# Kernel tuning notes

Hardware: AMD Instinct MI355X
Metric: run time of the kernel (lower is better)

The kernel has to match this reference:

```python
import jax, jax.numpy as jnp
import numpy as np

N, E, H = 25000, 100000, 32          # nodes, edges, node/clique hidden dim
NC, A, EC = 8000, 50000, 24000       # cliques, node2clique assignments, clique edges
EEMB, CEE, L = 8, 8, 2               # edge emb dims, n layers


def segment_mean(vals, ids, num):
    s = jax.ops.segment_sum(vals, ids, num_segments=num)
    cnt = jax.ops.segment_sum(jnp.ones(ids.shape[0], vals.dtype), ids, num_segments=num)
    return s / jnp.maximum(cnt, 1.0)[:, None]


def setup_inputs() -> dict:
    key = jax.random.key(0)
    ks = jax.random.split(key, 24)
    s = 0.1  # param scale
    inp = {
        "node_features": jax.random.normal(ks[0], (N, H), jnp.float32),
        "edge_index": jax.random.randint(ks[1], (2, E), 0, N),
        "edge_features": jax.random.normal(ks[2], (E, EEMB), jnp.float32),
        "clique_features": jax.random.normal(ks[3], (NC, H), jnp.float32),
        "node2clique_index": jnp.stack([
            jax.random.randint(ks[4], (A,), 0, N),
            jax.random.randint(ks[5], (A,), 0, NC)]),
        "clique_edge_index": jax.random.randint(ks[6], (2, EC), 0, NC),
        "clique_edge_features": jax.random.normal(ks[7], (EC, CEE), jnp.float32),
        # node NNConv params (stacked over L layers)
        "nn1_w": jax.random.normal(ks[8], (L, EEMB, H)) * s,
        "nn1_b": jnp.zeros((L, H)),
        "nn2_w": jax.random.normal(ks[9], (L, H, H * H)) * s,
        "nn2_b": jnp.zeros((L, H * H)),
        "root_w": jax.random.normal(ks[10], (L, H, H)) * s,
        "root_b": jnp.zeros((L, H)),
        # Node2Clique linear
        "n2c_w": jax.random.normal(ks[11], (L, H, H)) * s,
        "n2c_b": jnp.zeros((L, H)),
        # clique NNConv params
        "cnn1_w": jax.random.normal(ks[12], (L, CEE, H)) * s,
        "cnn1_b": jnp.zeros((L, H)),
        "cnn2_w": jax.random.normal(ks[13], (L, H, H * H)) * s,
        "cnn2_b": jnp.zeros((L, H * H)),
        "croot_w": jax.random.normal(ks[14], (L, H, H)) * s,
        "croot_b": jnp.zeros((L, H)),
        # Clique2Node linear
        "c2n_w": jax.random.normal(ks[15], (L, H, H)) * s,
        "c2n_b": jnp.zeros((L, H)),
    }
    return inp


def nnconv(x, src, dst, edge_attr, w1, b1, w2, b2, rw, rb, n_out_nodes):
    # per-edge weight matrices from the edge MLP: [E, in, out]
    h = jax.nn.relu(edge_attr @ w1 + b1)
    We = (h @ w2 + b2).reshape(edge_attr.shape[0], x.shape[1], -1)
    msg = jnp.einsum('ei,eio->eo', x[src], We)           # message from source
    agg = segment_mean(msg, dst, n_out_nodes)            # mean aggregation at target
    return agg + x @ rw + rb                             # root weight + bias


def reference(node_features, edge_index, edge_features, clique_features,
              node2clique_index, clique_edge_index, clique_edge_features,
              nn1_w, nn1_b, nn2_w, nn2_b, root_w, root_b, n2c_w, n2c_b,
              cnn1_w, cnn1_b, cnn2_w, cnn2_b, croot_w, croot_b, c2n_w, c2n_b):
    x, c = node_features, clique_features
    src, dst = edge_index[0], edge_index[1]
    nid, cid = node2clique_index[0], node2clique_index[1]
    csrc, cdst = clique_edge_index[0], clique_edge_index[1]
    for l in range(L):
        # node-level edge-conditioned conv
        x = jax.nn.relu(nnconv(x, src, dst, edge_features,
                               nn1_w[l], nn1_b[l], nn2_w[l], nn2_b[l],
                               root_w[l], root_b[l], N))
        # Node2Clique: project node feats, scatter-mean into cliques
        m = x @ n2c_w[l] + n2c_b[l]
        c = c + segment_mean(m[nid], cid, NC)
        # clique-level edge-conditioned conv
        c = jax.nn.relu(nnconv(c, csrc, cdst, clique_edge_features,
                               cnn1_w[l], cnn1_b[l], cnn2_w[l], cnn2_b[l],
                               croot_w[l], croot_b[l], NC))
        # Clique2Node: project clique feats, scatter-mean back onto nodes
        m = c @ c2n_w[l] + c2n_b[l]
        x = x + segment_mean(m[cid], nid, N)
    return (x, c)
```

## Files before the change

kernel.cpp:

```cpp
#include <hip/hip_runtime.h>
#include <hip/hip_bf16.h>

typedef unsigned int u32;
typedef unsigned short u16;

#define DEVINL __device__ __forceinline__

constexpr int Nn  = 25000;
constexpr int Ee  = 100000;
constexpr int NCc = 8000;
constexpr int Aa  = 50000;
constexpr int ECc = 24000;
constexpr int TCOLS = 1088;
constexpr int WPSZ  = TCOLS*32;
constexpr int TT_ROW = 561;
constexpr int NB_N = (Nn + 255)/256;
constexpr int NB_C = (NCc + 255)/256;
constexpr int PB_EN = (Ee + 255)/256;
constexpr int PB_EC = (ECc + 255)/256;
constexpr int PB_AS = (2*Aa + 255)/256;
constexpr int PB_WP = (4*WPSZ + 255)/256;

typedef float f32x4 __attribute__((ext_vector_type(4)));
typedef _Float16 h16x2 __attribute__((ext_vector_type(2)));
typedef _Float16 h16x8 __attribute__((ext_vector_type(8)));

DEVINL float b2f(u16 u){ union{u32 i;float f;}v; v.i = ((u32)u)<<16; return v.f; }
DEVINL float bfl(u32 u){ union{u32 i;float f;}v; v.i = u<<16; return v.f; }
DEVINL float bfh(u32 u){ union{u32 i;float f;}v; v.i = u & 0xffff0000u; return v.f; }
DEVINL u16 f2b(float f){ union{float f;u32 i;}v; v.f=f; u32 i=v.i;
  return (u16)((i + 0x7fffu + ((i>>16)&1u)) >> 16); }
DEVINL u16 f2h(float x){ union{ _Float16 h; u16 u; } v; v.h = (_Float16)x; return v.u; }
DEVINL u32 pkh2(float a, float b){
  union{ _Float16 h[2]; u32 u; } v;
  v.h[0] = (_Float16)a; v.h[1] = (_Float16)b; return v.u;
}
DEVINL float ldw(const void* p, long i, int f){
  return f ? ((const float*)p)[i] : b2f(((const u16*)p)[i]);
}
DEVINL float dot2f(u32 a, u32 b, float c){
  union U{u32 u; h16x2 h;};
  U ua; ua.u = a; U ub; ub.u = b;
#if __has_builtin(__builtin_amdgcn_fdot2)
  return __builtin_amdgcn_fdot2(ua.h, ub.h, c, false);
#else
  return c + (float)ua.h[0]*(float)ub.h[0] + (float)ua.h[1]*(float)ub.h[1];
#endif
}

__global__ __launch_bounds__(256) void k_detect_count(const u16* __restrict__ p, int n,
                        u32* __restrict__ maxbits, int* __restrict__ zcnt,
                        int* __restrict__ done, int* __restrict__ flag,
                        const int* __restrict__ ei, const int* __restrict__ cei,
                        const int* __restrict__ n2c,
                        int* __restrict__ deg_nd, int* __restrict__ deg_ce,
                        int* __restrict__ deg_n2c, int* __restrict__ deg_c2n,
                        int* __restrict__ cnt_sn, int* __restrict__ cnt_sc){
  int i0 = blockIdx.x*256 + threadIdx.x;
  { int t = i0;
    if (t < Ee)                             atomicAdd(&deg_nd[ei[Ee + t]], 1);
    else if ((t -= Ee) < ECc)               atomicAdd(&deg_ce[cei[ECc + t]], 1);
    else if ((t -= ECc) < Aa)               atomicAdd(&deg_n2c[n2c[Aa + t]], 1);
    else if ((t -= Aa) < Aa)                atomicAdd(&deg_c2n[n2c[t]], 1);
    else if ((t -= Aa) < Ee)                atomicAdd(&cnt_sn[ei[t]], 1);
    else if ((t -= Ee) < ECc)               atomicAdd(&cnt_sc[cei[t]], 1);
  }
  if (blockIdx.x >= 256) return;
  float lm = 0.f; int lz = 0;
  for (int i = i0; i < n; i += 256*256){
    u16 v = p[i];
    if (v == 0) lz++;
    lm = fmaxf(lm, fabsf(b2f(v)));
  }
  #pragma unroll
  for (int off = 32; off; off >>= 1){
    lm = fmaxf(lm, __shfl_down(lm, off));
    lz += __shfl_down(lz, off);
  }
  __shared__ float smax[4]; __shared__ int szc[4];
  if ((threadIdx.x & 63) == 0){
    smax[threadIdx.x >> 6] = lm;
    szc[threadIdx.x >> 6] = lz;
  }
  __syncthreads();
  if (threadIdx.x == 0){
    float m = fmaxf(fmaxf(smax[0], smax[1]), fmaxf(smax[2], smax[3]));
    int z = szc[0] + szc[1] + szc[2] + szc[3];
    atomicMax(maxbits, __float_as_uint(m));
    atomicAdd(zcnt, z);
    __threadfence();
    if (atomicAdd(done, 1) == 255){
      float mm = __uint_as_float(*maxbits);
      *flag = (mm > 1e6f || *zcnt > n/4) ? 1 : 0;
    }
  }
}

DEVINL void segof(int bid, int& seg, int& rb){
  seg = 0; rb = bid;
  while (true){
    int nb = (seg & 1) ? NB_C : NB_N;
    if (rb < nb) break;
    rb -= nb; seg++;
  }
}

__global__ __launch_bounds__(256) void k_scan_block6(
    const int* __restrict__ c0, const int* __restrict__ c1,
    const int* __restrict__ c2, const int* __restrict__ c3,
    const int* __restrict__ c4, const int* __restrict__ c5,
    int* __restrict__ o0, int* __restrict__ o1, int* __restrict__ o2,
    int* __restrict__ o3, int* __restrict__ o4, int* __restrict__ o5,
    int* __restrict__ b0, int* __restrict__ b1, int* __restrict__ b2,
    int* __restrict__ b3, int* __restrict__ b4, int* __restrict__ b5){
  __shared__ int s[256];
  int seg, rb; segof(blockIdx.x, seg, rb);
  const int* cnt; int* offs; int* bs;
  switch (seg){
    case 0: cnt=c0; offs=o0; bs=b0; break;
    case 1: cnt=c1; offs=o1; bs=b1; break;
    case 2: cnt=c2; offs=o2; bs=b2; break;
    case 3: cnt=c3; offs=o3; bs=b3; break;
    case 4: cnt=c4; offs=o4; bs=b4; break;
    default: cnt=c5; offs=o5; bs=b5; break;
  }
  int M = (seg & 1) ? NCc : Nn;
  int tid = threadIdx.x;
  int i = rb*256 + tid;
  int v = (i < M) ? cnt[i] : 0;
  s[tid] = v; __syncthreads();
  for (int d = 1; d < 256; d <<= 1){
    int t = (tid >= d) ? s[tid-d] : 0;
    __syncthreads();
    s[tid] += t;
    __syncthreads();
  }
  if (i < M) offs[i] = s[tid] - v;
  if (tid == 255) bs[rb] = s[255];
}

__global__ __launch_bounds__(256) void k_scan_fix6(
    int* __restrict__ o0, int* __restrict__ o1, int* __restrict__ o2,
    int* __restrict__ o3, int* __restrict__ o4, int* __restrict__ o5,
    const int* __restrict__ b0, const int* __restrict__ b1, const int* __restrict__ b2,
    const int* __restrict__ b3, const int* __restrict__ b4, const int* __restrict__ b5){
  __shared__ int s[256];
  int seg, rb; segof(blockIdx.x, seg, rb);
  int* offs; const int* bsp;
  switch (seg){
    case 0: offs=o0; bsp=b0; break;
    case 1: offs=o1; bsp=b1; break;
    case 2: offs=o2; bsp=b2; break;
    case 3: offs=o3; bsp=b3; break;
    case 4: offs=o4; bsp=b4; break;
    default: offs=o5; bsp=b5; break;
  }
  int M = (seg & 1) ? NCc : Nn;
  int tid = threadIdx.x;
  int v = (tid < rb) ? bsp[tid] : 0;
  s[tid] = v; __syncthreads();
  #pragma unroll
  for (int d = 128; d; d >>= 1){
    if (tid < d) s[tid] += s[tid + d];
    __syncthreads();
  }
  int prefix = s[0];
  int i = rb*256 + tid;
  if (i < M) offs[i] += prefix;
}

__global__ __launch_bounds__(256) void k_place_pack(
    const int* __restrict__ ei, const int* __restrict__ cei, const int* __restrict__ n2c,
    const void* __restrict__ ef, const void* __restrict__ cef,
    const void* __restrict__ nn1w, const void* __restrict__ nn1b,
    const void* __restrict__ cnn1w, const void* __restrict__ cnn1b,
    const void* __restrict__ nn2w, const void* __restrict__ nn2b, const void* __restrict__ rootw,
    const void* __restrict__ cnn2w, const void* __restrict__ cnn2b, const void* __restrict__ crootw,
    const int* __restrict__ offs_n, const int* __restrict__ offs_c,
    const int* __restrict__ offs_an, const int* __restrict__ offs_ac,
    const int* __restrict__ doffs_n, const int* __restrict__ doffs_c,
    int* __restrict__ cur_n, int* __restrict__ cur_c,
    int* __restrict__ cur_an, int* __restrict__ cur_ac,
    int* __restrict__ cur_dn, int* __restrict__ cur_dc,
    int2* __restrict__ sdp_n, int2* __restrict__ sdp_c,
    u32* __restrict__ hp_n, u32* __restrict__ hp_c,
    int* __restrict__ an2c, int* __restrict__ ac2n,
    const int* __restrict__ flag, u16* __restrict__ Wp4){
  int b = blockIdx.x, tid = threadIdx.x;
  int f = *flag;
  if (b < PB_EN + PB_EC){
    __shared__ float w1s[2][256], b1s[2][32];
    int isC = (b >= PB_EN);
    int e = (isC ? b - PB_EN : b)*256 + tid;
    int E = isC ? ECc : Ee;
    const void* W1 = isC ? cnn1w : nn1w;
    const void* B1 = isC ? cnn1b : nn1b;
    w1s[0][tid] = ldw(W1, tid, f);
    w1s[1][tid] = ldw(W1, 256 + tid, f);
    if (tid < 32){ b1s[0][tid] = ldw(B1, tid, f); b1s[1][tid] = ldw(B1, 32 + tid, f); }
    __syncthreads();
    if (e < E){
      const int* EI = isC ? cei : ei;
      int s = EI[e], d = EI[E + e];
      int* cur = isC ? cur_c : cur_n;
      const int* offs = isC ? offs_c : offs_n;
      int p = offs[s] + atomicAdd(&cur[s], 1);
      const int* dofs = isC ? doffs_c : doffs_n;
      int* curd = isC ? cur_dc : cur_dn;
      int dsl = dofs[d] + atomicAdd(&curd[d], 1);
      (isC ? sdp_c : sdp_n)[p] = make_int2(s, dsl);
      const void* EF = isC ? cef : ef;
      float ev[8];
      #pragma unroll
      for (int j = 0; j < 8; j++) ev[j] = ldw(EF, (long)e*8 + j, f);
      u32* hp = isC ? hp_c : hp_n;
      #pragma unroll
      for (int l = 0; l < 2; l++){
        u32* hq = hp + (size_t)l*E*16 + (size_t)p*16;
        #pragma unroll
        for (int kk = 0; kk < 16; kk++){
          float a0 = b1s[l][2*kk], a1 = b1s[l][2*kk+1];
          #pragma unroll
          for (int j = 0; j < 8; j++){
            a0 += ev[j]*w1s[l][j*32 + 2*kk];
            a1 += ev[j]*w1s[l][j*32 + 2*kk + 1];
          }
          hq[kk] = pkh2(fmaxf(a0, 0.f), fmaxf(a1, 0.f));
        }
      }
    }
  } else if (b < PB_EN + PB_EC + PB_AS){
    int i = (b - PB_EN - PB_EC)*256 + tid;
    if (i < Aa){
      int c = n2c[Aa + i];
      an2c[offs_ac[c] + atomicAdd(&cur_ac[c], 1)] = n2c[i];
    } else if ((i -= Aa) < Aa){
      int nd = n2c[i];
      ac2n[offs_an[nd] + atomicAdd(&cur_an[nd], 1)] = n2c[Aa + i];
    }
  } else {
    int i = (b - PB_EN - PB_EC - PB_AS)*256 + tid;
    if (i >= 4*WPSZ) return;
    int set = i / WPSZ, j = i - set*WPSZ;
    int l = set >> 1, isC = set & 1;
    const void* W2 = isC ? cnn2w : nn2w;
    const void* B2 = isC ? cnn2b : nn2b;
    const void* RW = isC ? crootw : rootw;
    int col = j >> 5, ii = j & 31;
    float v;
    if (col < 1024)      v = ldw(W2, (long)l*32768 + ((col>>5)<<10) + (ii<<5) + (col&31), f);
    else if (col < 1056) v = ldw(B2, (long)l*1024 + (ii<<5) + (col-1024), f);
    else                 v = ldw(RW, (long)l*1024 + (ii<<5) + (col-1056), f);
    Wp4[i] = f2h(v);
  }
}

__global__ __launch_bounds__(512) void k_conv_fused(const void* __restrict__ base, int braw,
                           const float* __restrict__ adm, const int* __restrict__ sidx,
                           const int* __restrict__ soffs, const int* __restrict__ sdeg, int M,
                           const int2* __restrict__ sdp, const u32* __restrict__ hp,
                           const int* __restrict__ offs, int E_,
                           const u16* __restrict__ Wp,
                           const void* __restrict__ rb, long rboff,
                           const int* __restrict__ flag,
                           float* __restrict__ feat_root, float* __restrict__ msg){
  __shared__ __align__(16) u32 Tt[16*TT_ROW];
  __shared__ __align__(16) u32 hws[8][64];
  int tid = threadIdx.x;
  int w = tid >> 6, lane = tid & 63;
  int quad = lane >> 4, lm = lane & 15;
  int n0 = blockIdx.x * 16;
  int f = *flag;
  int n = n0 + lm;
  int nc = n < M ? n : M-1;
  long bidx = (long)nc*32 + quad*8;
  float fv[8];
  if (braw && f == 0){
    uint4 q = *(const uint4*)((const u16*)base + bidx);
    fv[0]=bfl(q.x); fv[1]=bfh(q.x); fv[2]=bfl(q.y); fv[3]=bfh(q.y);
    fv[4]=bfl(q.z); fv[5]=bfh(q.z); fv[6]=bfl(q.w); fv[7]=bfh(q.w);
  } else {
    const float4* bp = (const float4*)((const float*)base + bidx);
    float4 q0 = bp[0], q1 = bp[1];
    fv[0]=q0.x; fv[1]=q0.y; fv[2]=q0.z; fv[3]=q0.w;
    fv[4]=q1.x; fv[5]=q1.y; fv[6]=q1.z; fv[7]=q1.w;
  }
  if (adm){
    int slo = soffs[nc], scnt = sdeg[nc];
    float ac[8] = {0,0,0,0,0,0,0,0};
    for (int k = 0; k < scnt; k++){
      const float4* mp = (const float4*)(adm + (size_t)sidx[slo + k]*32 + quad*8);
      float4 a0 = mp[0], a1 = mp[1];
      ac[0]+=a0.x; ac[1]+=a0.y; ac[2]+=a0.z; ac[3]+=a0.w;
      ac[4]+=a1.x; ac[5]+=a1.y; ac[6]+=a1.z; ac[7]+=a1.w;
    }
    float inv = 1.f/(float)(scnt > 1 ? scnt : 1);
    #pragma unroll
    for (int j = 0; j < 8; j++) fv[j] += ac[j]*inv;
  }
  union { h16x8 v; u32 u[4]; } bf;
  #pragma unroll
  for (int j = 0; j < 4; j++) bf.u[j] = pkh2(fv[2*j], fv[2*j+1]);

  #define AFR(ct) (*(const h16x8*)(Wp + (size_t)((ct)*16 + lm)*32 + quad*8))
  f32x4 z4 = {0.f, 0.f, 0.f, 0.f};
  #pragma unroll
  for (int g = 0; g < 2; g++){
    int q = w + 8*g;
    f32x4 c0 = __builtin_amdgcn_mfma_f32_16x16x32_f16(AFR(4*q+0), bf.v, z4, 0, 0, 0);
    f32x4 c1 = __builtin_amdgcn_mfma_f32_16x16x32_f16(AFR(4*q+1), bf.v, z4, 0, 0, 0);
    f32x4 c2 = __builtin_amdgcn_mfma_f32_16x16x32_f16(AFR(4*q+2), bf.v, z4, 0, 0, 0);
    f32x4 c3 = __builtin_amdgcn_mfma_f32_16x16x32_f16(AFR(4*q+3), bf.v, z4, 0, 0, 0);
    int rbase = lm*TT_ROW;
    int ob = quad*4;
    #pragma unroll
    for (int i = 0; i < 4; i++){
      Tt[rbase + (ob+i)*17 + q]      = pkh2(c0[i], c2[i]);
      Tt[rbase + (16+ob+i)*17 + q]   = pkh2(c1[i], c3[i]);
    }
  }
  if (w < 4){
    int ct = 64 + w;
    f32x4 c = __builtin_amdgcn_mfma_f32_16x16x32_f16(AFR(ct), bf.v, z4, 0, 0, 0);
    if (ct < 66){
      int p0 = (ct-64)*8 + quad*2;
      Tt[lm*TT_ROW + 544 + p0]     = pkh2(c[0], c[1]);
      Tt[lm*TT_ROW + 544 + p0 + 1] = pkh2(c[2], c[3]);
    } else if (n < M){
      int o = (ct-66)*16 + quad*4;
      float4 v = make_float4(c[0] + ldw(rb, rboff+o,   f),
                             c[1] + ldw(rb, rboff+o+1, f),
                             c[2] + ldw(rb, rboff+o+2, f),
                             c[3] + ldw(rb, rboff+o+3, f));
      *(float4*)&feat_root[(size_t)n*32 + o] = v;
    }
  }
  __syncthreads();

  int lo = offs[n0];
  int hi = (n0 + 16 < M) ? offs[n0 + 16] : E_;
  int eg = quad, kk = lm;
  int pos = lo + w*4;
  u32 hp0 = 0, hp1 = 0; int sd0 = 0, sd1 = 0;
  { int idx = pos*16 + lane;      if (idx < hi*16) hp0 = hp[idx];
    idx = (pos+32)*16 + lane;     if (idx < hi*16) hp1 = hp[idx]; }
  if (lane < 8){
    int idx = pos*2 + lane;       if (idx < hi*2) sd0 = ((const int*)sdp)[idx];
    idx = (pos+32)*2 + lane;      if (idx < hi*2) sd1 = ((const int*)sdp)[idx];
  }
  for (; pos < hi; pos += 32){
    int np = pos + 64;
    u32 hp2 = 0; int sd2 = 0;
    { int idx = np*16 + lane; if (idx < hi*16) hp2 = hp[idx]; }
    if (lane < 8){ int idx = np*2 + lane; if (idx < hi*2) sd2 = ((const int*)sdp)[idx]; }
    hws[w][lane] = hp0;
    int sn = __shfl(sd0, 2*eg);
    int ds = __shfl(sd0, 2*eg + 1);
    bool valid = (pos + eg < hi);
    int sr = sn - n0; sr = sr < 0 ? 0 : (sr > 15 ? 15 : sr);
    const u32* Tr = Tt + sr*TT_ROW;
    const u32* T0 = Tr + 34*kk;
    const uint4* Hp4 = (const uint4*)&hws[w][eg*16];
    union{u32 u; h16x2 h;} b2u; b2u.u = Tr[544 + kk];
    float m0 = (float)b2u.h[0], m1 = (float)b2u.h[1];
    #pragma unroll
    for (int g = 0; g < 4; g++){
      uint4 hv4 = Hp4[g];
      m0 = dot2f(hv4.x, T0[4*g+0], m0);  m1 = dot2f(hv4.x, T0[17+4*g+0], m1);
      m0 = dot2f(hv4.y, T0[4*g+1], m0);  m1 = dot2f(hv4.y, T0[17+4*g+1], m1);
      m0 = dot2f(hv4.z, T0[4*g+2], m0);  m1 = dot2f(hv4.z, T0[17+4*g+2], m1);
      m0 = dot2f(hv4.w, T0[4*g+3], m0);  m1 = dot2f(hv4.w, T0[17+4*g+3], m1);
    }
    if (valid){
      float* ap = msg + (size_t)ds*32 + 2*kk;
      ap[0] = m0;
      ap[1] = m1;
    }
    hp0 = hp1; sd0 = sd1; hp1 = hp2; sd1 = sd2;
  }
  #undef AFR
}

__global__ __launch_bounds__(256) void k_update_lin(const float* __restrict__ msg,
                           const int* __restrict__ doffs, const int* __restrict__ deg,
                           const float* __restrict__ feat_root, int M,
                           const void* __restrict__ w, long woff,
                           const void* __restrict__ b, long boff,
                           const int* __restrict__ flag,
                           float* __restrict__ feat, float* __restrict__ mout){
  __shared__ float wsm[1024], bs[32], rows[8][33];
  int tid = threadIdx.x;
  int f = *flag;
  for (int idx = tid; idx < 1024; idx += 256) wsm[idx] = ldw(w, woff + idx, f);
  if (tid < 32) bs[tid] = ldw(b, boff + tid, f);
  int nl = tid >> 5, o = tid & 31;
  int n = blockIdx.x*8 + nl;
  long i = (long)n*32 + o;
  if (n < M){
    int lo = doffs[n], dg = deg[n];
    float a = 0.f;
    for (int k = 0; k < dg; k++) a += msg[(size_t)(lo + k)*32 + o];
    float d = (float)(dg > 1 ? dg : 1);
    float v = fmaxf(a/d + feat_root[i], 0.f);
    rows[nl][o] = v;
    feat[i] = v;
  }
  __syncthreads();
  if (n >= M) return;
  float acc = bs[o];
  #pragma unroll
  for (int j = 0; j < 32; j++) acc += rows[nl][j]*wsm[j*32+o];
  mout[i] = acc;
}

__global__ __launch_bounds__(256) void k_store(const float* __restrict__ x,
                      const float* __restrict__ mC, const int* __restrict__ sidx,
                      const int* __restrict__ soffs, const int* __restrict__ sdeg,
                      const float* __restrict__ c,
                      void* __restrict__ out, const int* __restrict__ flag){
  int i = blockIdx.x*256 + threadIdx.x;
  int tot = Nn*32 + NCc*32;
  if (i >= tot) return;
  float v;
  if (i < Nn*32){
    int n = i >> 5, o = i & 31;
    int lo = soffs[n], dg = sdeg[n];
    float a = 0.f;
    for (int k = 0; k < dg; k++) a += mC[(size_t)sidx[lo + k]*32 + o];
    v = x[i] + a/(float)(dg > 1 ? dg : 1);
  } else v = c[i - Nn*32];
  if (*flag) ((float*)out)[i] = v;
  else       ((u16*)out)[i]   = f2b(v);
}

extern "C" void kernel_launch(void* const* d_in, const int* in_sizes, int n_in,
                              void* d_out, int out_size, void* d_ws, size_t ws_size,
                              hipStream_t stream){
  const int* ei  = (const int*)d_in[1];
  const int* n2c = (const int*)d_in[4];
  const int* cei = (const int*)d_in[5];
  const void *efr = d_in[2], *cefr = d_in[6];
  const void *nn1w = d_in[7], *nn1b = d_in[8], *nn2w = d_in[9], *nn2b = d_in[10],
             *rootw = d_in[11], *rootb = d_in[12], *n2cw = d_in[13], *n2cb = d_in[14],
             *cnn1w = d_in[15], *cnn1b = d_in[16], *cnn2w = d_in[17], *cnn2b = d_in[18],
             *crootw = d_in[19], *crootb = d_in[20], *c2nw = d_in[21], *c2nb = d_in[22];

  char* ws = (char*)d_ws;
  size_t off = 0;
  auto alloc = [&](size_t bytes){ void* p = ws + off; off += (bytes + 255) & ~(size_t)255; return p; };

  size_t zstart = off;
  int* deg_nd  = (int*)alloc((size_t)Nn*4);
  int* deg_ce  = (int*)alloc((size_t)NCc*4);
  int* deg_n2c = (int*)alloc((size_t)NCc*4);
  int* deg_c2n = (int*)alloc((size_t)Nn*4);
  int* cnt_sn  = (int*)alloc((size_t)Nn*4);
  int* cnt_sc  = (int*)alloc((size_t)NCc*4);
  int* cur_n   = (int*)alloc((size_t)Nn*4);
  int* cur_c   = (int*)alloc((size_t)NCc*4);
  int* cur_an  = (int*)alloc((size_t)Nn*4);
  int* cur_ac  = (int*)alloc((size_t)NCc*4);
  int* cur_dn  = (int*)alloc((size_t)Nn*4);
  int* cur_dc  = (int*)alloc((size_t)NCc*4);
  u32* maxbits = (u32*)alloc(256);
  int* zcnt = (int*)((char*)maxbits + 4);
  int* flag = (int*)((char*)maxbits + 8);
  int* done = (int*)((char*)maxbits + 12);
  size_t zbytes = off - zstart;

  float* xB  = (float*)alloc((size_t)Nn*32*4);
  float* xC  = (float*)alloc((size_t)Nn*32*4);
  float* cC0 = (float*)alloc((size_t)NCc*32*4);
  float* cC1 = (float*)alloc((size_t)NCc*32*4);
  float* frn = (float*)alloc((size_t)Nn*32*4);
  float* frc = (float*)alloc((size_t)NCc*32*4);
  float* msgN = (float*)alloc((size_t)Ee*32*4);
  float* msgC = (float*)alloc((size_t)ECc*32*4);
  float* mN  = (float*)alloc((size_t)Nn*32*4);
  float* mC  = (float*)alloc((size_t)NCc*32*4);
  int* offs_n  = (int*)alloc((size_t)Nn*4);
  int* offs_c  = (int*)alloc((size_t)NCc*4);
  int* offs_an = (int*)alloc((size_t)Nn*4);
  int* offs_ac = (int*)alloc((size_t)NCc*4);
  int* doffs_n = (int*)alloc((size_t)Nn*4);
  int* doffs_c = (int*)alloc((size_t)NCc*4);
  int* bs0 = (int*)alloc(512); int* bs1 = (int*)alloc(512);
  int* bs2 = (int*)alloc(512); int* bs3 = (int*)alloc(512);
  int* bs4 = (int*)alloc(512); int* bs5 = (int*)alloc(512);
  int* an2c = (int*)alloc((size_t)Aa*4);
  int* ac2n = (int*)alloc((size_t)Aa*4);
  int2* sdp_n = (int2*)alloc((size_t)Ee*8);
  int2* sdp_c = (int2*)alloc((size_t)ECc*8);
  u16* Wp4 = (u16*)alloc((size_t)4*WPSZ*2);
  u32* hp_n = (u32*)alloc((size_t)2*Ee*16*4);
  u32* hp_c = (u32*)alloc((size_t)2*ECc*16*4);

  auto nb = [](int n){ return (n + 255)/256; };

  hipMemsetAsync(ws + zstart, 0, zbytes, stream);
  k_detect_count<<<nb(2*Ee + 2*ECc + 2*Aa),256,0,stream>>>((const u16*)d_in[0], Nn*32,
      maxbits, zcnt, done, flag, ei, cei, n2c,
      deg_nd, deg_ce, deg_n2c, deg_c2n, cnt_sn, cnt_sc);
  k_scan_block6<<<3*(NB_N+NB_C),256,0,stream>>>(cnt_sn, cnt_sc, deg_c2n, deg_n2c, deg_nd, deg_ce,
      offs_n, offs_c, offs_an, offs_ac, doffs_n, doffs_c,
      bs0, bs1, bs2, bs3, bs4, bs5);
  k_scan_fix6<<<3*(NB_N+NB_C),256,0,stream>>>(offs_n, offs_c, offs_an, offs_ac, doffs_n, doffs_c,
      bs0, bs1, bs2, bs3, bs4, bs5);
  k_place_pack<<<PB_EN+PB_EC+PB_AS+PB_WP,256,0,stream>>>(ei, cei, n2c, efr, cefr,
      nn1w, nn1b, cnn1w, cnn1b, nn2w, nn2b, rootw, cnn2w, cnn2b, crootw,
      offs_n, offs_c, offs_an, offs_ac, doffs_n, doffs_c,
      cur_n, cur_c, cur_an, cur_ac, cur_dn, cur_dc,
      sdp_n, sdp_c, hp_n, hp_c, an2c, ac2n, flag, Wp4);

  int Gn = (Nn + 15)/16, Gc = (NCc + 15)/16;

  k_conv_fused<<<Gn,512,0,stream>>>(d_in[0], 1, nullptr, nullptr, nullptr, nullptr, Nn,
      sdp_n, hp_n, offs_n, Ee, Wp4 + 0*WPSZ, rootb, 0, flag, frn, msgN);
  k_update_lin<<<(Nn+7)/8,256,0,stream>>>(msgN, doffs_n, deg_nd, frn, Nn,
      n2cw, 0, n2cb, 0, flag, xB, mN);
  k_conv_fused<<<Gc,512,0,stream>>>(d_in[3], 1, mN, an2c, offs_ac, deg_n2c, NCc,
      sdp_c, hp_c, offs_c, ECc, Wp4 + 1*WPSZ, crootb, 0, flag, frc, msgC);
  k_update_lin<<<(NCc+7)/8,256,0,stream>>>(msgC, doffs_c, deg_ce, frc, NCc,
      c2nw, 0, c2nb, 0, flag, cC0, mC);
  k_conv_fused<<<Gn,512,0,stream>>>(xB, 0, mC, ac2n, offs_an, deg_c2n, Nn,
      sdp_n, hp_n + (size_t)Ee*16, offs_n, Ee, Wp4 + 2*WPSZ, rootb, 32, flag, frn, msgN);
  k_update_lin<<<(Nn+7)/8,256,0,stream>>>(msgN, doffs_n, deg_nd, frn, Nn,
      n2cw, 1024, n2cb, 32, flag, xC, mN);
  k_conv_fused<<<Gc,512,0,stream>>>(cC0, 0, mN, an2c, offs_ac, deg_n2c, NCc,
      sdp_c, hp_c + (size_t)ECc*16, offs_c, ECc, Wp4 + 3*WPSZ, crootb, 32, flag, frc, msgC);
  k_update_lin<<<(NCc+7)/8,256,0,stream>>>(msgC, doffs_c, deg_ce, frc, NCc,
      c2nw, 1024, c2nb, 32, flag, cC1, mC);
  k_store<<<nb(Nn*32 + NCc*32),256,0,stream>>>(xC, mC, ac2n, offs_an, deg_c2n, cC1, d_out, flag);
}
```

Measured before the change: 289.3 us.

## Fuse layer kernels into one persistent kernel with software grid barriers

```diff
diff --git a/kernel.cpp b/kernel.cpp
--- a/kernel.cpp
+++ b/kernel.cpp
@@ -20,6 +20,11 @@
 constexpr int PB_EC = (ECc + 255)/256;
 constexpr int PB_AS = (2*Aa + 255)/256;
 constexpr int PB_WP = (4*WPSZ + 255)/256;
+constexpr int NBLK = 512;
+constexpr int LTH  = 512;
+constexpr int NBAR = 8;
+constexpr int GV_N = (Nn + 15)/16;
+constexpr int GV_C = (NCc + 15)/16;
 
 typedef float f32x4 __attribute__((ext_vector_type(4)));
 typedef _Float16 h16x2 __attribute__((ext_vector_type(2)));
@@ -255,22 +260,32 @@
   }
 }
 
-__global__ __launch_bounds__(512) void k_conv_fused(const void* __restrict__ base, int braw,
-                           const float* __restrict__ adm, const int* __restrict__ sidx,
-                           const int* __restrict__ soffs, const int* __restrict__ sdeg, int M,
-                           const int2* __restrict__ sdp, const u32* __restrict__ hp,
-                           const int* __restrict__ offs, int E_,
-                           const u16* __restrict__ Wp,
-                           const void* __restrict__ rb, long rboff,
-                           const int* __restrict__ flag,
-                           float* __restrict__ feat_root, float* __restrict__ msg){
-  __shared__ __align__(16) u32 Tt[16*TT_ROW];
-  __shared__ __align__(16) u32 hws[8][64];
+DEVINL void gbar(int* gc, int* rc, int* fl, int id){
+  __syncthreads();
+  if (threadIdx.x == 0){
+    __threadfence();
+    int g = blockIdx.x & 7;
+    int* gcp = gc + (id*8 + g)*32;
+    if (atomicAdd(gcp, 1) == (NBLK/8) - 1){
+      if (atomicAdd(rc + id*32, 1) == 7)
+        __hip_atomic_store(fl + id*32, 1, __ATOMIC_RELEASE, __HIP_MEMORY_SCOPE_AGENT);
+    }
+    while (!__hip_atomic_load(fl + id*32, __ATOMIC_RELAXED, __HIP_MEMORY_SCOPE_AGENT))
+      __builtin_amdgcn_s_sleep(2);
+    (void)__hip_atomic_load(fl + id*32, __ATOMIC_ACQUIRE, __HIP_MEMORY_SCOPE_AGENT);
+  }
+  __syncthreads();
+}
+
+DEVINL void conv_phase(int v, const void* base, int braw,
+    const float* adm, const int* sidx, const int* soffs, const int* sdeg, int M,
+    const int2* sdp, const u32* hp, const int* offs, int E_,
+    const u16* Wp, const void* rb, long rboff, int f,
+    float* feat_root, float* msg, u32* Tt, u32* hws){
   int tid = threadIdx.x;
   int w = tid >> 6, lane = tid & 63;
   int quad = lane >> 4, lm = lane & 15;
-  int n0 = blockIdx.x * 16;
-  int f = *flag;
+  int n0 = v * 16;
   int n = n0 + lm;
   int nc = n < M ? n : M-1;
   long bidx = (long)nc*32 + quad*8;
@@ -328,11 +343,11 @@
       Tt[lm*TT_ROW + 544 + p0 + 1] = pkh2(c[2], c[3]);
     } else if (n < M){
       int o = (ct-66)*16 + quad*4;
-      float4 v = make_float4(c[0] + ldw(rb, rboff+o,   f),
-                             c[1] + ldw(rb, rboff+o+1, f),
-                             c[2] + ldw(rb, rboff+o+2, f),
-                             c[3] + ldw(rb, rboff+o+3, f));
-      *(float4*)&feat_root[(size_t)n*32 + o] = v;
+      float4 vv = make_float4(c[0] + ldw(rb, rboff+o,   f),
+                              c[1] + ldw(rb, rboff+o+1, f),
+                              c[2] + ldw(rb, rboff+o+2, f),
+                              c[3] + ldw(rb, rboff+o+3, f));
+      *(float4*)&feat_root[(size_t)n*32 + o] = vv;
     }
   }
   __syncthreads();
@@ -348,19 +363,20 @@
     int idx = pos*2 + lane;       if (idx < hi*2) sd0 = ((const int*)sdp)[idx];
     idx = (pos+32)*2 + lane;      if (idx < hi*2) sd1 = ((const int*)sdp)[idx];
   }
+  u32* hwsw = hws + w*64;
   for (; pos < hi; pos += 32){
     int np = pos + 64;
     u32 hp2 = 0; int sd2 = 0;
     { int idx = np*16 + lane; if (idx < hi*16) hp2 = hp[idx]; }
     if (lane < 8){ int idx = np*2 + lane; if (idx < hi*2) sd2 = ((const int*)sdp)[idx]; }
-    hws[w][lane] = hp0;
+    hwsw[lane] = hp0;
     int sn = __shfl(sd0, 2*eg);
     int ds = __shfl(sd0, 2*eg + 1);
     bool valid = (pos + eg < hi);
     int sr = sn - n0; sr = sr < 0 ? 0 : (sr > 15 ? 15 : sr);
     const u32* Tr = Tt + sr*TT_ROW;
     const u32* T0 = Tr + 34*kk;
-    const uint4* Hp4 = (const uint4*)&hws[w][eg*16];
+    const uint4* Hp4 = (const uint4*)&hwsw[eg*16];
     union{u32 u; h16x2 h;} b2u; b2u.u = Tr[544 + kk];
     float m0 = (float)b2u.h[0], m1 = (float)b2u.h[1];
     #pragma unroll
@@ -379,58 +395,104 @@
     hp0 = hp1; sd0 = sd1; hp1 = hp2; sd1 = sd2;
   }
   #undef AFR
-}
-
-__global__ __launch_bounds__(256) void k_update_lin(const float* __restrict__ msg,
-                           const int* __restrict__ doffs, const int* __restrict__ deg,
-                           const float* __restrict__ feat_root, int M,
-                           const void* __restrict__ w, long woff,
-                           const void* __restrict__ b, long boff,
-                           const int* __restrict__ flag,
-                           float* __restrict__ feat, float* __restrict__ mout){
-  __shared__ float wsm[1024], bs[32], rows[8][33];
+  __syncthreads();
+}
+
+DEVINL void upd_phase(int nvb, const float* msg, const int* doffs, const int* deg,
+    const float* froot, int M, const void* w_, long woff, const void* b_, long boff,
+    int f, float* feat, float* mout, char* smem){
+  float* wsm = (float*)smem;
+  float* bsv = wsm + 1024;
+  float (*rows)[33] = (float(*)[33])(bsv + 32);
+  int tid = threadIdx.x;
+  for (int idx = tid; idx < 1024; idx += LTH) wsm[idx] = ldw(w_, woff + idx, f);
+  if (tid < 32) bsv[tid] = ldw(b_, boff + tid, f);
+  __syncthreads();
+  int nl = tid >> 5, o = tid & 31;
+  for (int v = blockIdx.x; v < nvb; v += NBLK){
+    int n = v*16 + nl;
+    long i = (long)n*32 + o;
+    if (n < M){
+      int lo = doffs[n], dg = deg[n];
+      float a = 0.f;
+      for (int k = 0; k < dg; k++) a += msg[(size_t)(lo + k)*32 + o];
+      float d = (float)(dg > 1 ? dg : 1);
+      float val = fmaxf(a/d + froot[i], 0.f);
+      rows[nl][o] = val;
+      feat[i] = val;
+    }
+    __syncthreads();
+    if (n < M){
+      float acc = bsv[o];
+      #pragma unroll
+      for (int j = 0; j < 32; j++) acc += rows[nl][j]*wsm[j*32+o];
+      mout[i] = acc;
+    }
+    __syncthreads();
+  }
+}
+
+__global__ __launch_bounds__(512, 4) void k_layers(
+    const int* __restrict__ flag, const u16* __restrict__ Wp4,
+    const int2* __restrict__ sdp_n, const u32* __restrict__ hp_n,
+    const int* __restrict__ offs_n, const int* __restrict__ doffs_n, const int* __restrict__ deg_nd,
+    const int2* __restrict__ sdp_c, const u32* __restrict__ hp_c,
+    const int* __restrict__ offs_c, const int* __restrict__ doffs_c, const int* __restrict__ deg_ce,
+    const int* __restrict__ an2c, const int* __restrict__ offs_ac, const int* __restrict__ deg_n2c,
+    const int* __restrict__ ac2n, const int* __restrict__ offs_an, const int* __restrict__ deg_c2n,
+    const void* __restrict__ rootb, const void* __restrict__ n2cw, const void* __restrict__ n2cb,
+    const void* __restrict__ crootb, const void* __restrict__ c2nw, const void* __restrict__ c2nb,
+    const void* __restrict__ x_in, const void* __restrict__ c_in,
+    float* __restrict__ frn, float* __restrict__ frc,
+    float* __restrict__ msgN, float* __restrict__ msgC,
+    float* __restrict__ xB, float* __restrict__ xC,
+    float* __restrict__ cC0, float* __restrict__ cC1,
+    float* __restrict__ mN, float* __restrict__ mC,
+    void* __restrict__ out,
+    int* __restrict__ bgc, int* __restrict__ brc, int* __restrict__ bfl){
+  __shared__ __align__(16) char smem[37952];
+  u32* Tt  = (u32*)smem;
+  u32* hws = (u32*)(smem + 16*TT_ROW*4);
   int tid = threadIdx.x;
   int f = *flag;
-  for (int idx = tid; idx < 1024; idx += 256) wsm[idx] = ldw(w, woff + idx, f);
-  if (tid < 32) bs[tid] = ldw(b, boff + tid, f);
-  int nl = tid >> 5, o = tid & 31;
-  int n = blockIdx.x*8 + nl;
-  long i = (long)n*32 + o;
-  if (n < M){
-    int lo = doffs[n], dg = deg[n];
-    float a = 0.f;
-    for (int k = 0; k < dg; k++) a += msg[(size_t)(lo + k)*32 + o];
-    float d = (float)(dg > 1 ? dg : 1);
-    float v = fmaxf(a/d + feat_root[i], 0.f);
-    rows[nl][o] = v;
-    feat[i] = v;
-  }
-  __syncthreads();
-  if (n >= M) return;
-  float acc = bs[o];
-  #pragma unroll
-  for (int j = 0; j < 32; j++) acc += rows[nl][j]*wsm[j*32+o];
-  mout[i] = acc;
-}
-
-__global__ __launch_bounds__(256) void k_store(const float* __restrict__ x,
-                      const float* __restrict__ mC, const int* __restrict__ sidx,
-                      const int* __restrict__ soffs, const int* __restrict__ sdeg,
-                      const float* __restrict__ c,
-                      void* __restrict__ out, const int* __restrict__ flag){
-  int i = blockIdx.x*256 + threadIdx.x;
+
+  for (int v = blockIdx.x; v < GV_N; v += NBLK)
+    conv_phase(v, x_in, 1, nullptr, nullptr, nullptr, nullptr, Nn,
+               sdp_n, hp_n, offs_n, Ee, Wp4, rootb, 0, f, frn, msgN, Tt, hws);
+  gbar(bgc, brc, bfl, 0);
+  upd_phase(GV_N, msgN, doffs_n, deg_nd, frn, Nn, n2cw, 0, n2cb, 0, f, xB, mN, smem);
+  gbar(bgc, brc, bfl, 1);
+  for (int v = blockIdx.x; v < GV_C; v += NBLK)
+    conv_phase(v, c_in, 1, mN, an2c, offs_ac, deg_n2c, NCc,
+               sdp_c, hp_c, offs_c, ECc, Wp4 + 1*WPSZ, crootb, 0, f, frc, msgC, Tt, hws);
+  gbar(bgc, brc, bfl, 2);
+  upd_phase(GV_C, msgC, doffs_c, deg_ce, frc, NCc, c2nw, 0, c2nb, 0, f, cC0, mC, smem);
+  gbar(bgc, brc, bfl, 3);
+  for (int v = blockIdx.x; v < GV_N; v += NBLK)
+    conv_phase(v, xB, 0, mC, ac2n, offs_an, deg_c2n, Nn,
+               sdp_n, hp_n + (size_t)Ee*16, offs_n, Ee, Wp4 + 2*WPSZ, rootb, 32, f, frn, msgN, Tt, hws);
+  gbar(bgc, brc, bfl, 4);
+  upd_phase(GV_N, msgN, doffs_n, deg_nd, frn, Nn, n2cw, 1024, n2cb, 32, f, xC, mN, smem);
+  gbar(bgc, brc, bfl, 5);
+  for (int v = blockIdx.x; v < GV_C; v += NBLK)
+    conv_phase(v, cC0, 0, mN, an2c, offs_ac, deg_n2c, NCc,
+               sdp_c, hp_c + (size_t)ECc*16, offs_c, ECc, Wp4 + 3*WPSZ, crootb, 32, f, frc, msgC, Tt, hws);
+  gbar(bgc, brc, bfl, 6);
+  upd_phase(GV_C, msgC, doffs_c, deg_ce, frc, NCc, c2nw, 1024, c2nb, 32, f, cC1, mC, smem);
+  gbar(bgc, brc, bfl, 7);
   int tot = Nn*32 + NCc*32;
-  if (i >= tot) return;
-  float v;
-  if (i < Nn*32){
-    int n = i >> 5, o = i & 31;
-    int lo = soffs[n], dg = sdeg[n];
-    float a = 0.f;
-    for (int k = 0; k < dg; k++) a += mC[(size_t)sidx[lo + k]*32 + o];
-    v = x[i] + a/(float)(dg > 1 ? dg : 1);
-  } else v = c[i - Nn*32];
-  if (*flag) ((float*)out)[i] = v;
-  else       ((u16*)out)[i]   = f2b(v);
+  for (int i = blockIdx.x*LTH + tid; i < tot; i += NBLK*LTH){
+    float v;
+    if (i < Nn*32){
+      int n = i >> 5, o = i & 31;
+      int lo = offs_an[n], dg = deg_c2n[n];
+      float a = 0.f;
+      for (int k = 0; k < dg; k++) a += mC[(size_t)ac2n[lo + k]*32 + o];
+      v = xC[i] + a/(float)(dg > 1 ? dg : 1);
+    } else v = cC1[i - Nn*32];
+    if (f) ((float*)out)[i] = v;
+    else   ((u16*)out)[i]   = f2b(v);
+  }
 }
 
 extern "C" void kernel_launch(void* const* d_in, const int* in_sizes, int n_in,
@@ -462,6 +524,9 @@
   int* cur_ac  = (int*)alloc((size_t)NCc*4);
   int* cur_dn  = (int*)alloc((size_t)Nn*4);
   int* cur_dc  = (int*)alloc((size_t)NCc*4);
+  int* bgc = (int*)alloc((size_t)NBAR*8*32*4);
+  int* brc = (int*)alloc((size_t)NBAR*32*4);
+  int* bfl = (int*)alloc((size_t)NBAR*32*4);
   u32* maxbits = (u32*)alloc(256);
   int* zcnt = (int*)((char*)maxbits + 4);
   int* flag = (int*)((char*)maxbits + 8);
@@ -511,24 +576,12 @@
       offs_n, offs_c, offs_an, offs_ac, doffs_n, doffs_c,
       cur_n, cur_c, cur_an, cur_ac, cur_dn, cur_dc,
       sdp_n, sdp_c, hp_n, hp_c, an2c, ac2n, flag, Wp4);
-
-  int Gn = (Nn + 15)/16, Gc = (NCc + 15)/16;
-
-  k_conv_fused<<<Gn,512,0,stream>>>(d_in[0], 1, nullptr, nullptr, nullptr, nullptr, Nn,
-      sdp_n, hp_n, offs_n, Ee, Wp4 + 0*WPSZ, rootb, 0, flag, frn, msgN);
-  k_update_lin<<<(Nn+7)/8,256,0,stream>>>(msgN, doffs_n, deg_nd, frn, Nn,
-      n2cw, 0, n2cb, 0, flag, xB, mN);
-  k_conv_fused<<<Gc,512,0,stream>>>(d_in[3], 1, mN, an2c, offs_ac, deg_n2c, NCc,
-      sdp_c, hp_c, offs_c, ECc, Wp4 + 1*WPSZ, crootb, 0, flag, frc, msgC);
-  k_update_lin<<<(NCc+7)/8,256,0,stream>>>(msgC, doffs_c, deg_ce, frc, NCc,
-      c2nw, 0, c2nb, 0, flag, cC0, mC);
-  k_conv_fused<<<Gn,512,0,stream>>>(xB, 0, mC, ac2n, offs_an, deg_c2n, Nn,
-      sdp_n, hp_n + (size_t)Ee*16, offs_n, Ee, Wp4 + 2*WPSZ, rootb, 32, flag, frn, msgN);
-  k_update_lin<<<(Nn+7)/8,256,0,stream>>>(msgN, doffs_n, deg_nd, frn, Nn,
-      n2cw, 1024, n2cb, 32, flag, xC, mN);
-  k_conv_fused<<<Gc,512,0,stream>>>(cC0, 0, mN, an2c, offs_ac, deg_n2c, NCc,
-      sdp_c, hp_c + (size_t)ECc*16, offs_c, ECc, Wp4 + 3*WPSZ, crootb, 32, flag, frc, msgC);
-  k_update_lin<<<(NCc+7)/8,256,0,stream>>>(msgC, doffs_c, deg_ce, frc, NCc,
-      c2nw, 1024, c2nb, 32, flag, cC1, mC);
-  k_store<<<nb(Nn*32 + NCc*32),256,0,stream>>>(xC, mC, ac2n, offs_an, deg_c2n, cC1, d_out, flag);
-}
+  k_layers<<<NBLK,LTH,0,stream>>>(flag, Wp4,
+      sdp_n, hp_n, offs_n, doffs_n, deg_nd,
+      sdp_c, hp_c, offs_c, doffs_c, deg_ce,
+      an2c, offs_ac, deg_n2c, ac2n, offs_an, deg_c2n,
+      rootb, n2cw, n2cb, crootb, c2nw, c2nb,
+      d_in[0], d_in[3],
+      frn, frc, msgN, msgC, xB, xC, cC0, cC1, mN, mC,
+      d_out, bgc, brc, bfl);
+}
```

Result: slower. 432.8 us (+49.6%).

## Store edge messages as fp16, merge scan kernels, write clique output directly

Applied to the files above, without the earlier changes.

```diff
diff --git a/kernel.cpp b/kernel.cpp
--- a/kernel.cpp
+++ b/kernel.cpp
@@ -16,6 +16,7 @@
 constexpr int TT_ROW = 561;
 constexpr int NB_N = (Nn + 255)/256;
 constexpr int NB_C = (NCc + 255)/256;
+constexpr int NSEGB = 3*(NB_N + NB_C);
 constexpr int PB_EN = (Ee + 255)/256;
 constexpr int PB_EC = (ECc + 255)/256;
 constexpr int PB_AS = (2*Aa + 255)/256;
@@ -105,68 +106,45 @@
   }
 }
 
-__global__ __launch_bounds__(256) void k_scan_block6(
+__global__ __launch_bounds__(256) void k_scan1(
     const int* __restrict__ c0, const int* __restrict__ c1,
     const int* __restrict__ c2, const int* __restrict__ c3,
     const int* __restrict__ c4, const int* __restrict__ c5,
     int* __restrict__ o0, int* __restrict__ o1, int* __restrict__ o2,
-    int* __restrict__ o3, int* __restrict__ o4, int* __restrict__ o5,
-    int* __restrict__ b0, int* __restrict__ b1, int* __restrict__ b2,
-    int* __restrict__ b3, int* __restrict__ b4, int* __restrict__ b5){
+    int* __restrict__ o3, int* __restrict__ o4, int* __restrict__ o5){
   __shared__ int s[256];
+  __shared__ int red[256];
   int seg, rb; segof(blockIdx.x, seg, rb);
-  const int* cnt; int* offs; int* bs;
+  const int* cnt; int* offs;
   switch (seg){
-    case 0: cnt=c0; offs=o0; bs=b0; break;
-    case 1: cnt=c1; offs=o1; bs=b1; break;
-    case 2: cnt=c2; offs=o2; bs=b2; break;
-    case 3: cnt=c3; offs=o3; bs=b3; break;
-    case 4: cnt=c4; offs=o4; bs=b4; break;
-    default: cnt=c5; offs=o5; bs=b5; break;
+    case 0: cnt=c0; offs=o0; break;
+    case 1: cnt=c1; offs=o1; break;
+    case 2: cnt=c2; offs=o2; break;
+    case 3: cnt=c3; offs=o3; break;
+    case 4: cnt=c4; offs=o4; break;
+    default: cnt=c5; offs=o5; break;
   }
   int M = (seg & 1) ? NCc : Nn;
-  int tid = threadIdx.x;
-  int i = rb*256 + tid;
-  int v = (i < M) ? cnt[i] : 0;
-  s[tid] = v; __syncthreads();
-  for (int d = 1; d < 256; d <<= 1){
-    int t = (tid >= d) ? s[tid-d] : 0;
-    __syncthreads();
-    s[tid] += t;
-    __syncthreads();
-  }
-  if (i < M) offs[i] = s[tid] - v;
-  if (tid == 255) bs[rb] = s[255];
-}
-
-__global__ __launch_bounds__(256) void k_scan_fix6(
-    int* __restrict__ o0, int* __restrict__ o1, int* __restrict__ o2,
-    int* __restrict__ o3, int* __restrict__ o4, int* __restrict__ o5,
-    const int* __restrict__ b0, const int* __restrict__ b1, const int* __restrict__ b2,
-    const int* __restrict__ b3, const int* __restrict__ b4, const int* __restrict__ b5){
-  __shared__ int s[256];
-  int seg, rb; segof(blockIdx.x, seg, rb);
-  int* offs; const int* bsp;
-  switch (seg){
-    case 0: offs=o0; bsp=b0; break;
-    case 1: offs=o1; bsp=b1; break;
-    case 2: offs=o2; bsp=b2; break;
-    case 3: offs=o3; bsp=b3; break;
-    case 4: offs=o4; bsp=b4; break;
-    default: offs=o5; bsp=b5; break;
-  }
-  int M = (seg & 1) ? NCc : Nn;
-  int tid = threadIdx.x;
-  int v = (tid < rb) ? bsp[tid] : 0;
-  s[tid] = v; __syncthreads();
+  int t = threadIdx.x;
+  int part = 0;
+  for (int j = t; j < rb*256; j += 256) part += cnt[j];
+  red[t] = part; __syncthreads();
   #pragma unroll
   for (int d = 128; d; d >>= 1){
-    if (tid < d) s[tid] += s[tid + d];
+    if (t < d) red[t] += red[t + d];
     __syncthreads();
   }
-  int prefix = s[0];
-  int i = rb*256 + tid;
-  if (i < M) offs[i] += prefix;
+  int prefix = red[0];
+  int i = rb*256 + t;
+  int v = (i < M) ? cnt[i] : 0;
+  s[t] = v; __syncthreads();
+  for (int d = 1; d < 256; d <<= 1){
+    int tv = (t >= d) ? s[t-d] : 0;
+    __syncthreads();
+    s[t] += tv;
+    __syncthreads();
+  }
+  if (i < M) offs[i] = prefix + s[t] - v;
 }
 
 __global__ __launch_bounds__(256) void k_place_pack(
@@ -263,7 +241,7 @@
                            const u16* __restrict__ Wp,
                            const void* __restrict__ rb, long rboff,
                            const int* __restrict__ flag,
-                           float* __restrict__ feat_root, float* __restrict__ msg){
+                           float* __restrict__ feat_root, u32* __restrict__ msgp){
   __shared__ __align__(16) u32 Tt[16*TT_ROW];
   __shared__ __align__(16) u32 hws[8][64];
   int tid = threadIdx.x;
@@ -372,22 +350,21 @@
       m0 = dot2f(hv4.w, T0[4*g+3], m0);  m1 = dot2f(hv4.w, T0[17+4*g+3], m1);
     }
     if (valid){
-      float* ap = msg + (size_t)ds*32 + 2*kk;
-      ap[0] = m0;
-      ap[1] = m1;
+      msgp[(size_t)ds*16 + kk] = pkh2(m0, m1);
     }
     hp0 = hp1; sd0 = sd1; hp1 = hp2; sd1 = sd2;
   }
   #undef AFR
 }
 
-__global__ __launch_bounds__(256) void k_update_lin(const float* __restrict__ msg,
+__global__ __launch_bounds__(256) void k_update_lin(const u32* __restrict__ msgp,
                            const int* __restrict__ doffs, const int* __restrict__ deg,
                            const float* __restrict__ feat_root, int M,
                            const void* __restrict__ w, long woff,
                            const void* __restrict__ b, long boff,
                            const int* __restrict__ flag,
-                           float* __restrict__ feat, float* __restrict__ mout){
+                           float* __restrict__ feat, float* __restrict__ mout,
+                           void* __restrict__ outp){
   __shared__ float wsm[1024], bs[32], rows[8][33];
   int tid = threadIdx.x;
   int f = *flag;
@@ -399,11 +376,20 @@
   if (n < M){
     int lo = doffs[n], dg = deg[n];
     float a = 0.f;
-    for (int k = 0; k < dg; k++) a += msg[(size_t)(lo + k)*32 + o];
+    for (int k = 0; k < dg; k++){
+      union{u32 u; h16x2 h;} c;
+      c.u = msgp[(size_t)(lo + k)*16 + (o >> 1)];
+      a += (float)c.h[o & 1];
+    }
     float d = (float)(dg > 1 ? dg : 1);
     float v = fmaxf(a/d + feat_root[i], 0.f);
     rows[nl][o] = v;
     feat[i] = v;
+    if (outp){
+      long oi = (long)Nn*32 + i;
+      if (f) ((float*)outp)[oi] = v;
+      else   ((u16*)outp)[oi]   = f2b(v);
+    }
   }
   __syncthreads();
   if (n >= M) return;
@@ -416,19 +402,14 @@
 __global__ __launch_bounds__(256) void k_store(const float* __restrict__ x,
                       const float* __restrict__ mC, const int* __restrict__ sidx,
                       const int* __restrict__ soffs, const int* __restrict__ sdeg,
-                      const float* __restrict__ c,
                       void* __restrict__ out, const int* __restrict__ flag){
   int i = blockIdx.x*256 + threadIdx.x;
-  int tot = Nn*32 + NCc*32;
-  if (i >= tot) return;
-  float v;
-  if (i < Nn*32){
-    int n = i >> 5, o = i & 31;
-    int lo = soffs[n], dg = sdeg[n];
-    float a = 0.f;
-    for (int k = 0; k < dg; k++) a += mC[(size_t)sidx[lo + k]*32 + o];
-    v = x[i] + a/(float)(dg > 1 ? dg : 1);
-  } else v = c[i - Nn*32];
+  if (i >= Nn*32) return;
+  int n = i >> 5, o = i & 31;
+  int lo = soffs[n], dg = sdeg[n];
+  float a = 0.f;
+  for (int k = 0; k < dg; k++) a += mC[(size_t)sidx[lo + k]*32 + o];
+  float v = x[i] + a/(float)(dg > 1 ? dg : 1);
   if (*flag) ((float*)out)[i] = v;
   else       ((u16*)out)[i]   = f2b(v);
 }
@@ -474,8 +455,8 @@
   float* cC1 = (float*)alloc((size_t)NCc*32*4);
   float* frn = (float*)alloc((size_t)Nn*32*4);
   float* frc = (float*)alloc((size_t)NCc*32*4);
-  float* msgN = (float*)alloc((size_t)Ee*32*4);
-  float* msgC = (float*)alloc((size_t)ECc*32*4);
+  u32* msgN = (u32*)alloc((size_t)Ee*16*4);
+  u32* msgC = (u32*)alloc((size_t)ECc*16*4);
   float* mN  = (float*)alloc((size_t)Nn*32*4);
   float* mC  = (float*)alloc((size_t)NCc*32*4);
   int* offs_n  = (int*)alloc((size_t)Nn*4);
@@ -484,9 +465,6 @@
   int* offs_ac = (int*)alloc((size_t)NCc*4);
   int* doffs_n = (int*)alloc((size_t)Nn*4);
   int* doffs_c = (int*)alloc((size_t)NCc*4);
-  int* bs0 = (int*)alloc(512); int* bs1 = (int*)alloc(512);
-  int* bs2 = (int*)alloc(512); int* bs3 = (int*)alloc(512);
-  int* bs4 = (int*)alloc(512); int* bs5 = (int*)alloc(512);
   int* an2c = (int*)alloc((size_t)Aa*4);
   int* ac2n = (int*)alloc((size_t)Aa*4);
   int2* sdp_n = (int2*)alloc((size_t)Ee*8);
@@ -501,11 +479,8 @@
   k_detect_count<<<nb(2*Ee + 2*ECc + 2*Aa),256,0,stream>>>((const u16*)d_in[0], Nn*32,
       maxbits, zcnt, done, flag, ei, cei, n2c,
       deg_nd, deg_ce, deg_n2c, deg_c2n, cnt_sn, cnt_sc);
-  k_scan_block6<<<3*(NB_N+NB_C),256,0,stream>>>(cnt_sn, cnt_sc, deg_c2n, deg_n2c, deg_nd, deg_ce,
-      offs_n, offs_c, offs_an, offs_ac, doffs_n, doffs_c,
-      bs0, bs1, bs2, bs3, bs4, bs5);
-  k_scan_fix6<<<3*(NB_N+NB_C),256,0,stream>>>(offs_n, offs_c, offs_an, offs_ac, doffs_n, doffs_c,
-      bs0, bs1, bs2, bs3, bs4, bs5);
+  k_scan1<<<NSEGB,256,0,stream>>>(cnt_sn, cnt_sc, deg_c2n, deg_n2c, deg_nd, deg_ce,
+      offs_n, offs_c, offs_an, offs_ac, doffs_n, doffs_c);
   k_place_pack<<<PB_EN+PB_EC+PB_AS+PB_WP,256,0,stream>>>(ei, cei, n2c, efr, cefr,
       nn1w, nn1b, cnn1w, cnn1b, nn2w, nn2b, rootw, cnn2w, cnn2b, crootw,
       offs_n, offs_c, offs_an, offs_ac, doffs_n, doffs_c,
@@ -517,18 +492,18 @@
   k_conv_fused<<<Gn,512,0,stream>>>(d_in[0], 1, nullptr, nullptr, nullptr, nullptr, Nn,
       sdp_n, hp_n, offs_n, Ee, Wp4 + 0*WPSZ, rootb, 0, flag, frn, msgN);
   k_update_lin<<<(Nn+7)/8,256,0,stream>>>(msgN, doffs_n, deg_nd, frn, Nn,
-      n2cw, 0, n2cb, 0, flag, xB, mN);
+      n2cw, 0, n2cb, 0, flag, xB, mN, nullptr);
   k_conv_fused<<<Gc,512,0,stream>>>(d_in[3], 1, mN, an2c, offs_ac, deg_n2c, NCc,
       sdp_c, hp_c, offs_c, ECc, Wp4 + 1*WPSZ, crootb, 0, flag, frc, msgC);
   k_update_lin<<<(NCc+7)/8,256,0,stream>>>(msgC, doffs_c, deg_ce, frc, NCc,
-      c2nw, 0, c2nb, 0, flag, cC0, mC);
+      c2nw, 0, c2nb, 0, flag, cC0, mC, nullptr);
   k_conv_fused<<<Gn,512,0,stream>>>(xB, 0, mC, ac2n, offs_an, deg_c2n, Nn,
       sdp_n, hp_n + (size_t)Ee*16, offs_n, Ee, Wp4 + 2*WPSZ, rootb, 32, flag, frn, msgN);
   k_update_lin<<<(Nn+7)/8,256,0,stream>>>(msgN, doffs_n, deg_nd, frn, Nn,
-      n2cw, 1024, n2cb, 32, flag, xC, mN);
+      n2cw, 1024, n2cb, 32, flag, xC, mN, nullptr);
   k_conv_fused<<<Gc,512,0,stream>>>(cC0, 0, mN, an2c, offs_ac, deg_n2c, NCc,
       sdp_c, hp_c + (size_t)ECc*16, offs_c, ECc, Wp4 + 3*WPSZ, crootb, 32, flag, frc, msgC);
   k_update_lin<<<(NCc+7)/8,256,0,stream>>>(msgC, doffs_c, deg_ce, frc, NCc,
-      c2nw, 1024, c2nb, 32, flag, cC1, mC);
-  k_store<<<nb(Nn*32 + NCc*32),256,0,stream>>>(xC, mC, ac2n, offs_an, deg_c2n, cC1, d_out, flag);
-}
+      c2nw, 1024, c2nb, 32, flag, cC1, mC, d_out);
+  k_store<<<nb(Nn*32),256,0,stream>>>(xC, mC, ac2n, offs_an, deg_c2n, d_out, flag);
+}
```

Measured after the change: 291.8 us. Within noise of the previous version (+0.9%).
